# Kernel tuning notes

Hardware: AMD Instinct MI355X
Metric: run time of the kernel (lower is better)

Reference implementation:

```python
import jax, jax.numpy as jnp
import numpy as np

B, L, H, V = 16, 512, 256, 32000
HALF = H // 2
EPS_LN = 1e-5
EPS_NORM = 1e-12


def setup_inputs() -> dict:
    key = jax.random.key(0)
    ks = jax.random.split(key, 9)
    s = 0.02
    return {
        "seq": jax.random.randint(ks[0], (B, L), 0, V),
        "embed": jax.random.normal(ks[1], (V, H), jnp.float32) * s,
        "W1": jax.random.normal(ks[2], (2 * H, H), jnp.float32) * s,
        "b1": jnp.zeros((2 * H,), jnp.float32),
        "W2": jax.random.normal(ks[3], (H, 2 * H), jnp.float32) * s,
        "b2": jnp.zeros((H,), jnp.float32),
        "gamma": jnp.ones((H,), jnp.float32),
        "beta": jnp.zeros((H,), jnp.float32),
        "W_sem": jax.random.normal(ks[4], (HALF, H), jnp.float32) * s,
        "W_epi": jax.random.normal(ks[5], (HALF, H), jnp.float32) * s,
        "W_rp": jax.random.normal(ks[6], (H, H), jnp.float32) * s,
        "b_rp": jnp.zeros((H,), jnp.float32),
        "W_out": jax.random.normal(ks[7], (V, H), jnp.float32) * s,
        "b_out": jnp.zeros((V,), jnp.float32),
    }


def _l2norm(x):
    # F.normalize(dim=-1): x / max(||x||, eps)
    n = jnp.sqrt(jnp.sum(x * x, axis=-1, keepdims=True))
    return x / jnp.maximum(n, EPS_NORM)


def reference(seq, embed, W1, b1, W2, b2, gamma, beta, W_sem, W_epi, W_rp, b_rp, W_out, b_out):
    h = embed[seq]                                   # [B, L, H]
    ff = jnp.maximum(h @ W1.T + b1, 0.0) @ W2.T + b2  # MLP with 2H hidden
    x = h + ff
    mu = jnp.mean(x, axis=-1, keepdims=True)
    var = jnp.var(x, axis=-1, keepdims=True)
    h = (x - mu) / jnp.sqrt(var + EPS_LN) * gamma + beta  # LayerNorm

    ks_all = jnp.einsum('blh,kh->blk', h, W_sem)     # [B, L, HALF]
    ke_all = jnp.einsum('blh,kh->blk', h, W_epi)

    def step(carry, kv):
        M_s, M_e = carry
        k_s, k_e = kv                                 # [B, HALF] each
        kns = _l2norm(k_s)
        kne = _l2norm(k_e)
        vps = jnp.einsum('bij,bj->bi', M_s, kns)      # read from fast weights
        vpe = jnp.einsum('bij,bj->bi', M_e, kne)
        M_s = M_s + jnp.einsum('bi,bj->bij', k_s - vps, kns)  # delta-rule write
        M_e = M_e + jnp.einsum('bi,bj->bij', k_e - vpe, kne)
        return (M_s, M_e), None

    M0 = jnp.zeros((B, HALF, HALF), h.dtype)
    # scan over timesteps 0..L-2 (time-major)
    (M_s, M_e), _ = jax.lax.scan(
        step, (M0, M0),
        (jnp.swapaxes(ks_all[:, :-1], 0, 1), jnp.swapaxes(ke_all[:, :-1], 0, 1)))

    cs = jnp.einsum('bij,bj->bi', M_s, ks_all[:, -1])  # read with last-token query
    ce = jnp.einsum('bij,bj->bi', M_e, ke_all[:, -1])
    c = jnp.concatenate([cs, ce], axis=-1)             # [B, H]
    r = c @ W_rp.T + b_rp
    return r @ W_out.T + b_out                          # [B, V]
```

## Files before the change

### kernel.cpp

```cpp
#include <hip/hip_runtime.h>

#define B_ 16
#define L_ 512
#define H_ 256
#define V_ 32000
#define HALF_ 128

typedef __attribute__((ext_vector_type(8))) short short8;
typedef __attribute__((ext_vector_type(4))) float floatx4;
typedef __attribute__((ext_vector_type(2))) float float2v;

__device__ __forceinline__ unsigned short f2bf(float x) {
  unsigned int u = __float_as_uint(x);
  unsigned int r = (u + 0x7FFFu + ((u >> 16) & 1u)) >> 16;
  return (unsigned short)r;
}

template <int CTRL>
__device__ __forceinline__ float dpp_xor_add(float x) {
  int y = __builtin_amdgcn_mov_dpp(__float_as_int(x), CTRL, 0xf, 0xf, true);
  return x + __int_as_float(y);
}

__device__ __forceinline__ float redu16(float p) {
  p = dpp_xor_add<0xB1>(p);
  p = dpp_xor_add<0x4E>(p);
  p = dpp_xor_add<0x141>(p);
  p = dpp_xor_add<0x140>(p);
  return p;
}

__device__ __forceinline__ float2v pk_fma(float2v a, float2v b, float2v c) {
  float2v d;
  asm("v_pk_fma_f32 %0, %1, %2, %3" : "=v"(d) : "v"(a), "v"(b), "v"(c));
  return d;
}
__device__ __forceinline__ float2v pk_mul(float2v a, float2v b) {
  float2v d;
  asm("v_pk_mul_f32 %0, %1, %2" : "=v"(d) : "v"(a), "v"(b));
  return d;
}

__device__ __forceinline__ void async_cp16(const float* g, float* l) {
  __builtin_amdgcn_global_load_lds(
      (const __attribute__((address_space(1))) void*)g,
      (__attribute__((address_space(3))) void*)l, 16, 0, 0);
}

__device__ __forceinline__ uint4 load8cvt(const float* p) {
  float4 a = ((const float4*)p)[0];
  float4 b = ((const float4*)p)[1];
  uint4 r;
  r.x = (unsigned)f2bf(a.x) | ((unsigned)f2bf(a.y) << 16);
  r.y = (unsigned)f2bf(a.z) | ((unsigned)f2bf(a.w) << 16);
  r.z = (unsigned)f2bf(b.x) | ((unsigned)f2bf(b.y) << 16);
  r.w = (unsigned)f2bf(b.z) | ((unsigned)f2bf(b.w) << 16);
  return r;
}

__global__ __launch_bounds__(256) void prep_kernel(const float* __restrict__ W1,
                                                   const float* __restrict__ W2,
                                                   const float* __restrict__ Ws,
                                                   const float* __restrict__ We,
                                                   unsigned short* __restrict__ W1b,
                                                   unsigned short* __restrict__ W2b,
                                                   unsigned short* __restrict__ Wcb) {
  int i = blockIdx.x * 256 + threadIdx.x;
  if (i < 131072) W1b[i] = f2bf(W1[i]);
  else if (i < 262144) W2b[i - 131072] = f2bf(W2[i - 131072]);
  else if (i < 294912) Wcb[i - 262144] = f2bf(Ws[i - 262144]);
  else Wcb[i - 262144] = f2bf(We[i - 294912]);
}

__global__ __launch_bounds__(256) void gemm1_kernel(const int* __restrict__ seq,
                                                    const float* __restrict__ embed,
                                                    const unsigned short* __restrict__ W1b,
                                                    const float* __restrict__ b1,
                                                    unsigned short* __restrict__ a1b) {
  __shared__ unsigned short As[128 * 40];
  __shared__ unsigned short Bs[128 * 40];
  int tid = threadIdx.x;
  int wave = tid >> 6, lane = tid & 63;
  int wm = (wave >> 1) * 64, wn = (wave & 1) * 64;
  int quad = lane >> 4, l15 = lane & 15;
  int bm = blockIdx.y * 128, bn = blockIdx.x * 128;
  int sr = tid >> 2, sq = tid & 3;

  int tok0 = seq[bm + sr];
  int tok1 = seq[bm + 64 + sr];

  floatx4 zero = {0.f, 0.f, 0.f, 0.f};
  floatx4 acc[4][4];
#pragma unroll
  for (int fi = 0; fi < 4; fi++)
#pragma unroll
    for (int fj = 0; fj < 4; fj++) acc[fi][fj] = zero;

  uint4 av0 = load8cvt(embed + (size_t)tok0 * H_ + sq * 8);
  uint4 av1 = load8cvt(embed + (size_t)tok1 * H_ + sq * 8);
  uint4 bv0 = *(const uint4*)(W1b + (size_t)(bn + sr) * 256 + sq * 8);
  uint4 bv1 = *(const uint4*)(W1b + (size_t)(bn + 64 + sr) * 256 + sq * 8);

  for (int k0 = 0; k0 < 256; k0 += 32) {
    __syncthreads();
    *(uint4*)(As + sr * 40 + sq * 8) = av0;
    *(uint4*)(As + (64 + sr) * 40 + sq * 8) = av1;
    *(uint4*)(Bs + sr * 40 + sq * 8) = bv0;
    *(uint4*)(Bs + (64 + sr) * 40 + sq * 8) = bv1;
    __syncthreads();
    if (k0 + 32 < 256) {
      av0 = load8cvt(embed + (size_t)tok0 * H_ + k0 + 32 + sq * 8);
      av1 = load8cvt(embed + (size_t)tok1 * H_ + k0 + 32 + sq * 8);
      bv0 = *(const uint4*)(W1b + (size_t)(bn + sr) * 256 + k0 + 32 + sq * 8);
      bv1 = *(const uint4*)(W1b + (size_t)(bn + 64 + sr) * 256 + k0 + 32 + sq * 8);
    }
    short8 af[4], bf[4];
#pragma unroll
    for (int f = 0; f < 4; f++) {
      af[f] = *(const short8*)(As + (wm + f * 16 + l15) * 40 + quad * 8);
      bf[f] = *(const short8*)(Bs + (wn + f * 16 + l15) * 40 + quad * 8);
    }
#pragma unroll
    for (int fi = 0; fi < 4; fi++)
#pragma unroll
      for (int fj = 0; fj < 4; fj++)
        acc[fi][fj] = __builtin_amdgcn_mfma_f32_16x16x32_bf16(af[fi], bf[fj], acc[fi][fj], 0, 0, 0);
  }

#pragma unroll
  for (int fi = 0; fi < 4; fi++) {
#pragma unroll
    for (int fj = 0; fj < 4; fj++) {
      int col = bn + wn + fj * 16 + l15;
      float bb = b1[col];
#pragma unroll
      for (int rg = 0; rg < 4; rg++) {
        int row = bm + wm + fi * 16 + quad * 4 + rg;
        float v = fmaxf(acc[fi][fj][rg] + bb, 0.f);
        a1b[(size_t)row * 512 + col] = f2bf(v);
      }
    }
  }
}

__global__ __launch_bounds__(256) void mlpk_kernel(const unsigned short* __restrict__ a1b,
                                                   const unsigned short* __restrict__ W2b,
                                                   const float* __restrict__ b2,
                                                   const int* __restrict__ seq,
                                                   const float* __restrict__ embed,
                                                   const float* __restrict__ gamma,
                                                   const float* __restrict__ beta,
                                                   const unsigned short* __restrict__ Wcb,
                                                   float* __restrict__ khat,
                                                   float* __restrict__ kT) {
  __shared__ unsigned short As[32 * 40];
  __shared__ unsigned short Bs[256 * 40];
  __shared__ unsigned short hnS[32 * 264];
  __shared__ float stats[2][2][32];
  int tid = threadIdx.x;
  int wave = tid >> 6, lane = tid & 63;
  int wm = (wave >> 1) * 16, wnh = wave & 1, wn = wnh * 128;
  int quad = lane >> 4, l15 = lane & 15;
  int bm = blockIdx.x * 32;
  int sr = tid >> 2, sq = tid & 3;

  floatx4 zero = {0.f, 0.f, 0.f, 0.f};
  floatx4 acc[8];
#pragma unroll
  for (int fj = 0; fj < 8; fj++) acc[fj] = zero;

  uint4 av, bv[4];
  if (tid < 128) av = *(const uint4*)(a1b + (size_t)(bm + sr) * 512 + sq * 8);
#pragma unroll
  for (int q = 0; q < 4; q++) {
    int unit = q * 256 + tid;
    bv[q] = *(const uint4*)(W2b + (size_t)(unit >> 2) * 512 + (unit & 3) * 8);
  }
  for (int k0 = 0; k0 < 512; k0 += 32) {
    __syncthreads();
    if (tid < 128) *(uint4*)(As + sr * 40 + sq * 8) = av;
#pragma unroll
    for (int q = 0; q < 4; q++) {
      int unit = q * 256 + tid;
      *(uint4*)(Bs + (unit >> 2) * 40 + (unit & 3) * 8) = bv[q];
    }
    __syncthreads();
    if (k0 + 32 < 512) {
      if (tid < 128) av = *(const uint4*)(a1b + (size_t)(bm + sr) * 512 + k0 + 32 + sq * 8);
#pragma unroll
      for (int q = 0; q < 4; q++) {
        int unit = q * 256 + tid;
        bv[q] = *(const uint4*)(W2b + (size_t)(unit >> 2) * 512 + k0 + 32 + (unit & 3) * 8);
      }
    }
    short8 af = *(const short8*)(As + (wm + l15) * 40 + quad * 8);
    short8 bf[8];
#pragma unroll
    for (int fj = 0; fj < 8; fj++)
      bf[fj] = *(const short8*)(Bs + (wn + fj * 16 + l15) * 40 + quad * 8);
#pragma unroll
    for (int fj = 0; fj < 8; fj++)
      acc[fj] = __builtin_amdgcn_mfma_f32_16x16x32_bf16(af, bf[fj], acc[fj], 0, 0, 0);
  }

  int seqv[4];
#pragma unroll
  for (int rg = 0; rg < 4; rg++) seqv[rg] = seq[bm + wm + quad * 4 + rg];
  float v[8][4];
#pragma unroll
  for (int fj = 0; fj < 8; fj++) {
    int col = wn + fj * 16 + l15;
    float bb = b2[col];
#pragma unroll
    for (int rg = 0; rg < 4; rg++)
      v[fj][rg] = acc[fj][rg] + bb + embed[(size_t)seqv[rg] * H_ + col];
  }
  float s_[4], q_[4];
#pragma unroll
  for (int rg = 0; rg < 4; rg++) {
    float s = 0.f, q = 0.f;
#pragma unroll
    for (int fj = 0; fj < 8; fj++) {
      s += v[fj][rg];
      q += v[fj][rg] * v[fj][rg];
    }
    s_[rg] = redu16(s);
    q_[rg] = redu16(q);
  }
  if (l15 == 0) {
#pragma unroll
    for (int rg = 0; rg < 4; rg++) {
      int rlocal = wm + quad * 4 + rg;
      stats[wnh][0][rlocal] = s_[rg];
      stats[wnh][1][rlocal] = q_[rg];
    }
  }
  __syncthreads();
#pragma unroll
  for (int rg = 0; rg < 4; rg++) {
    int rlocal = wm + quad * 4 + rg;
    float sum = stats[0][0][rlocal] + stats[1][0][rlocal];
    float ssq = stats[0][1][rlocal] + stats[1][1][rlocal];
    float mu = sum * (1.f / H_);
    float var = ssq * (1.f / H_) - mu * mu;
    float inv = rsqrtf(var + 1e-5f);
#pragma unroll
    for (int fj = 0; fj < 8; fj++) {
      int col = wn + fj * 16 + l15;
      float y = (v[fj][rg] - mu) * inv * gamma[col] + beta[col];
      hnS[rlocal * 264 + col] = f2bf(y);
    }
  }
  __syncthreads();

  floatx4 acc2[8];
#pragma unroll
  for (int fj = 0; fj < 8; fj++) acc2[fj] = zero;
#pragma unroll
  for (int q = 0; q < 4; q++) {
    int unit = q * 256 + tid;
    bv[q] = *(const uint4*)(Wcb + (size_t)(unit >> 2) * 256 + (unit & 3) * 8);
  }
  for (int k0 = 0; k0 < 256; k0 += 32) {
    __syncthreads();
#pragma unroll
    for (int q = 0; q < 4; q++) {
      int unit = q * 256 + tid;
      *(uint4*)(Bs + (unit >> 2) * 40 + (unit & 3) * 8) = bv[q];
    }
    __syncthreads();
    if (k0 + 32 < 256) {
#pragma unroll
      for (int q = 0; q < 4; q++) {
        int unit = q * 256 + tid;
        bv[q] = *(const uint4*)(Wcb + (size_t)(unit >> 2) * 256 + k0 + 32 + (unit & 3) * 8);
      }
    }
    short8 af = *(const short8*)(hnS + (wm + l15) * 264 + k0 + quad * 8);
    short8 bf[8];
#pragma unroll
    for (int fj = 0; fj < 8; fj++)
      bf[fj] = *(const short8*)(Bs + (wn + fj * 16 + l15) * 40 + quad * 8);
#pragma unroll
    for (int fj = 0; fj < 8; fj++)
      acc2[fj] = __builtin_amdgcn_mfma_f32_16x16x32_bf16(af, bf[fj], acc2[fj], 0, 0, 0);
  }

  int b = bm >> 9;
  int idxm = b * 2 + wnh;
  int tloc0 = (bm & 511) + wm + quad * 4;
  float inv[4];
#pragma unroll
  for (int rg = 0; rg < 4; rg++) {
    float ssq = 0.f;
#pragma unroll
    for (int fj = 0; fj < 8; fj++) ssq += acc2[fj][rg] * acc2[fj][rg];
    ssq = redu16(ssq);
    inv[rg] = 1.f / fmaxf(sqrtf(ssq), 1e-12f);
  }
#pragma unroll
  for (int fj = 0; fj < 8; fj++) {
    int ch = fj * 16 + l15;
    int j = ch >> 2, e = ch & 3;
    int pj = (j & 1) ? (16 + (j >> 1)) : (j >> 1);
    int pcol = pj * 4 + e;
#pragma unroll
    for (int rg = 0; rg < 4; rg++)
      khat[((size_t)idxm * L_ + tloc0 + rg) * HALF_ + pcol] = acc2[fj][rg] * inv[rg];
    float4 raw = {acc2[fj][0], acc2[fj][1], acc2[fj][2], acc2[fj][3]};
    *(float4*)(kT + (size_t)idxm * (HALF_ * L_) + (size_t)ch * L_ + tloc0) = raw;
  }
}

#define STEP(KP, KR)                                                     \
  do {                                                                   \
    float2v t_ = pk_mul(m01, KP[0]);                                     \
    t_ = pk_fma(m23, KP[1], t_);                                         \
    t_ = pk_fma(m45, KP[2], t_);                                         \
    t_ = pk_fma(m67, KP[3], t_);                                         \
    float p_ = t_.x + t_.y;                                              \
    p_ = redu16(p_);                                                     \
    float sv_ = (KR) - p_;                                               \
    float2v s2_ = {sv_, sv_};                                            \
    m01 = pk_fma(s2_, KP[0], m01);                                       \
    m23 = pk_fma(s2_, KP[1], m23);                                       \
    m45 = pk_fma(s2_, KP[2], m45);                                       \
    m67 = pk_fma(s2_, KP[3], m67);                                       \
  } while (0)

#define LOADPK(DST, PTR)                                                 \
  do {                                                                   \
    float4 a_ = *(const float4*)(PTR);                                   \
    float4 b_ = *(const float4*)((PTR) + 64);                            \
    DST[0] = (float2v){a_.x, a_.y};                                      \
    DST[1] = (float2v){a_.z, a_.w};                                      \
    DST[2] = (float2v){b_.x, b_.y};                                      \
    DST[3] = (float2v){b_.z, b_.w};                                      \
  } while (0)

__global__ __launch_bounds__(256) void scan_kernel(const float* __restrict__ khat,
                                                   const float* __restrict__ kT,
                                                   float* __restrict__ c) {
  __shared__ float sk[2][64 * 128];
  int bid = blockIdx.x;
  int idxm = bid & 31;
  int rg = bid >> 5;
  int b = idxm >> 1, mat = idxm & 1;
  const float* kh = khat + (size_t)idxm * L_ * HALF_;
  const float* kTi = kT + (size_t)idxm * HALF_ * L_;

  int tid = threadIdx.x;
  int wave = tid >> 6, lane = tid & 63;
  int seg = tid & 15, rl = tid >> 4;
  int r = rg * 16 + rl;
  int c0 = seg * 8;
  const float* krow = kTi + (size_t)r * L_;

  float2v m01 = {0.f, 0.f}, m23 = {0.f, 0.f}, m45 = {0.f, 0.f}, m67 = {0.f, 0.f};

#pragma unroll
  for (int j = 0; j < 8; j++)
    async_cp16(kh + wave * 2048 + j * 256 + lane * 4, &sk[0][wave * 2048 + j * 256] + lane * 4);
  __syncthreads();

  float4 krn = *(const float4*)(krow);
  const float* lb = &sk[0][0] + seg * 4;

  for (int ch = 0; ch < 7; ch++) {
#pragma unroll
    for (int j = 0; j < 8; j++)
      async_cp16(kh + (size_t)(ch + 1) * 8192 + wave * 2048 + j * 256 + lane * 4,
                 &sk[(ch + 1) & 1][wave * 2048 + j * 256] + lane * 4);
    const float* base = lb + (ch & 1) * 8192;
    float2v pk[4][4];
#pragma unroll
    for (int u = 0; u < 4; u++) LOADPK(pk[u], base + u * 128);
    for (int g = 0; g < 15; g++) {
      float4 krc = krn;
      krn = *(const float4*)(krow + ch * 64 + g * 4 + 4);
#pragma unroll
      for (int u = 0; u < 4; u++) {
        STEP(pk[u], ((u == 0) ? krc.x : (u == 1) ? krc.y : (u == 2) ? krc.z : krc.w));
        int tn = g * 4 + u + 4;
        LOADPK(pk[u], base + tn * 128);
      }
    }
    {
      float4 krc = krn;
      krn = *(const float4*)(krow + ch * 64 + 64);
      STEP(pk[0], krc.x);
      STEP(pk[1], krc.y);
      STEP(pk[2], krc.z);
      STEP(pk[3], krc.w);
    }
    __syncthreads();
  }

  {
    const float* base = lb + 8192;
    float2v pk[4][4];
#pragma unroll
    for (int u = 0; u < 4; u++) LOADPK(pk[u], base + u * 128);
    for (int g = 0; g < 15; g++) {
      float4 krc = krn;
      krn = *(const float4*)(krow + 448 + g * 4 + 4);
#pragma unroll
      for (int u = 0; u < 4; u++) {
        STEP(pk[u], ((u == 0) ? krc.x : (u == 1) ? krc.y : (u == 2) ? krc.z : krc.w));
        int tn = g * 4 + u + 4;
        LOADPK(pk[u], base + tn * 128);
      }
    }
    float4 krc = krn;
    STEP(pk[0], krc.x);
    STEP(pk[1], krc.y);
    STEP(pk[2], krc.z);
  }

  float q[8];
#pragma unroll
  for (int j = 0; j < 8; j++) q[j] = kTi[(size_t)(c0 + j) * L_ + 511];
  float t0 = m01.x * q[0] + m01.y * q[1];
  float t1 = m23.x * q[2] + m23.y * q[3];
  float t2 = m45.x * q[4] + m45.y * q[5];
  float t3 = m67.x * q[6] + m67.y * q[7];
  float p = redu16((t0 + t1) + (t2 + t3));
  if (seg == 0) c[(size_t)b * H_ + mat * HALF_ + r] = p;
}

__global__ void rp_kernel(const float* __restrict__ c, const float* __restrict__ Wrp,
                          const float* __restrict__ brp, float* __restrict__ r) {
  int b = blockIdx.x;
  int n = threadIdx.x;
  __shared__ float cs[H_];
  cs[n] = c[(size_t)b * H_ + n];
  __syncthreads();
  const float4* w4 = (const float4*)(Wrp + (size_t)n * H_);
  const float4* c4 = (const float4*)cs;
  float acc = 0.f;
#pragma unroll 8
  for (int k = 0; k < H_ / 4; k++) {
    float4 w = w4[k], cc = c4[k];
    acc += w.x * cc.x + w.y * cc.y + w.z * cc.z + w.w * cc.w;
  }
  r[(size_t)b * H_ + n] = acc + brp[n];
}

__global__ __launch_bounds__(256) void out_kernel(const float* __restrict__ r,
                                                  const float* __restrict__ Wout,
                                                  const float* __restrict__ bout,
                                                  float* __restrict__ out) {
  __shared__ float rs[16 * 272];
  __shared__ float obuf[16 * 68];
  int tid = threadIdx.x;
#pragma unroll
  for (int q = 0; q < 16; q++) {
    int idx = q * 256 + tid;
    int bb = idx >> 8, cc = idx & 255;
    rs[bb * 272 + cc + 4 * (cc >> 6)] = r[idx];
  }
  __syncthreads();
  int row = tid >> 2, part = tid & 3;
  int v = blockIdx.x * 64 + row;
  const float4* w4 = (const float4*)(Wout + (size_t)v * H_ + part * 64);
  float acc[16];
#pragma unroll
  for (int bb = 0; bb < 16; bb++) acc[bb] = 0.f;
#pragma unroll 4
  for (int j = 0; j < 16; j++) {
    float4 w = w4[j];
#pragma unroll
    for (int bb = 0; bb < 16; bb++) {
      float4 rv = *(const float4*)&rs[bb * 272 + part * 68 + j * 4];
      acc[bb] += w.x * rv.x + w.y * rv.y + w.z * rv.z + w.w * rv.w;
    }
  }
  float bo = bout[v];
#pragma unroll
  for (int bb = 0; bb < 16; bb++) {
    acc[bb] = dpp_xor_add<0xB1>(acc[bb]);
    acc[bb] = dpp_xor_add<0x4E>(acc[bb]);
  }
#pragma unroll
  for (int q = 0; q < 4; q++) {
    int bb = part * 4 + q;
    obuf[bb * 68 + row] = acc[bb] + bo;
  }
  __syncthreads();
#pragma unroll
  for (int q = 0; q < 4; q++) {
    int idx = q * 256 + tid;
    int bb = idx >> 6, vl = idx & 63;
    out[(size_t)bb * V_ + blockIdx.x * 64 + vl] = obuf[bb * 68 + vl];
  }
}

extern "C" void kernel_launch(void* const* d_in, const int* in_sizes, int n_in,
                              void* d_out, int out_size, void* d_ws, size_t ws_size,
                              hipStream_t stream) {
  const int* seq = (const int*)d_in[0];
  const float* embed = (const float*)d_in[1];
  const float* W1 = (const float*)d_in[2];
  const float* b1 = (const float*)d_in[3];
  const float* W2 = (const float*)d_in[4];
  const float* b2 = (const float*)d_in[5];
  const float* gamma = (const float*)d_in[6];
  const float* beta = (const float*)d_in[7];
  const float* Wsem = (const float*)d_in[8];
  const float* Wepi = (const float*)d_in[9];
  const float* Wrp = (const float*)d_in[10];
  const float* brp = (const float*)d_in[11];
  const float* Wout = (const float*)d_in[12];
  const float* bout = (const float*)d_in[13];
  float* out = (float*)d_out;

  float* ws = (float*)d_ws;
  unsigned short* a1b = (unsigned short*)ws;
  float* khat = ws + 2097152;
  float* kT = ws + 4194304;
  unsigned short* W1b = (unsigned short*)(ws + 6291456);
  unsigned short* W2b = (unsigned short*)(ws + 6356992);
  unsigned short* Wcb = (unsigned short*)(ws + 6422528);
  float* c = ws + 6455296;
  float* r = ws + 6459392;

  prep_kernel<<<1280, 256, 0, stream>>>(W1, W2, Wsem, Wepi, W1b, W2b, Wcb);
  gemm1_kernel<<<dim3(4, 64), 256, 0, stream>>>(seq, embed, W1b, b1, a1b);
  mlpk_kernel<<<256, 256, 0, stream>>>(a1b, W2b, b2, seq, embed, gamma, beta, Wcb, khat, kT);
  scan_kernel<<<256, 256, 0, stream>>>(khat, kT, c);
  rp_kernel<<<16, 256, 0, stream>>>(c, Wrp, brp, r);
  out_kernel<<<500, 256, 0, stream>>>(r, Wout, bout, out);
}
```

Baseline: 231.4 us.

## Replace transposed raw-key buffer with per-token norms, rebuilding raw keys from normalized keys

The MLP kernel no longer writes a transposed copy of the unnormalized keys. It writes only the per-token L2 norm, and its normalized-key output now goes through shared memory so global stores are coalesced float4 rows. The scan kernel rebuilds the raw key as normalized key times norm, reading the normalized key from the shared tile it already loads. The final query read reuses the last normalized key scaled by its norm. This removes a large global write and the strided raw-key reads, in exchange for an extra LDS read per step and more shared memory in the MLP kernel.

```diff
diff --git a/kernel.cpp b/kernel.cpp
--- a/kernel.cpp
+++ b/kernel.cpp
@@ -152,11 +152,12 @@
                                                    const float* __restrict__ beta,
                                                    const unsigned short* __restrict__ Wcb,
                                                    float* __restrict__ khat,
-                                                   float* __restrict__ kT) {
+                                                   float* __restrict__ nrm) {
   __shared__ unsigned short As[32 * 40];
   __shared__ unsigned short Bs[256 * 40];
   __shared__ unsigned short hnS[32 * 264];
   __shared__ float stats[2][2][32];
+  __shared__ float stg[2][32 * 132];
   int tid = threadIdx.x;
   int wave = tid >> 6, lane = tid & 63;
   int wm = (wave >> 1) * 16, wnh = wave & 1, wn = wnh * 128;
@@ -289,14 +290,19 @@
   int b = bm >> 9;
   int idxm = b * 2 + wnh;
   int tloc0 = (bm & 511) + wm + quad * 4;
-  float inv[4];
+  float inv[4], nr4[4];
 #pragma unroll
   for (int rg = 0; rg < 4; rg++) {
     float ssq = 0.f;
 #pragma unroll
     for (int fj = 0; fj < 8; fj++) ssq += acc2[fj][rg] * acc2[fj][rg];
     ssq = redu16(ssq);
-    inv[rg] = 1.f / fmaxf(sqrtf(ssq), 1e-12f);
+    nr4[rg] = fmaxf(sqrtf(ssq), 1e-12f);
+    inv[rg] = 1.f / nr4[rg];
+  }
+  if (l15 == 0) {
+#pragma unroll
+    for (int rg = 0; rg < 4; rg++) nrm[(size_t)idxm * L_ + tloc0 + rg] = nr4[rg];
   }
 #pragma unroll
   for (int fj = 0; fj < 8; fj++) {
@@ -304,15 +310,24 @@
     int j = ch >> 2, e = ch & 3;
     int pj = (j & 1) ? (16 + (j >> 1)) : (j >> 1);
     int pcol = pj * 4 + e;
+    int trl = wm + quad * 4;
 #pragma unroll
     for (int rg = 0; rg < 4; rg++)
-      khat[((size_t)idxm * L_ + tloc0 + rg) * HALF_ + pcol] = acc2[fj][rg] * inv[rg];
-    float4 raw = {acc2[fj][0], acc2[fj][1], acc2[fj][2], acc2[fj][3]};
-    *(float4*)(kT + (size_t)idxm * (HALF_ * L_) + (size_t)ch * L_ + tloc0) = raw;
-  }
-}
-
-#define STEP(KP, KR)                                                     \
+      stg[wnh][(trl + rg) * 132 + pcol] = acc2[fj][rg] * inv[rg];
+  }
+  __syncthreads();
+#pragma unroll
+  for (int f = 0; f < 8; f++) {
+    int idx = f * 256 + tid;
+    int w = idx >> 10, rem = idx & 1023;
+    int tr = rem >> 5, l = rem & 31;
+    float4 vv = *(float4*)&stg[w][tr * 132 + l * 4];
+    int im = (bm >> 9) * 2 + w;
+    *(float4*)&khat[((size_t)im * L_ + (bm & 511) + tr) * HALF_ + l * 4] = vv;
+  }
+}
+
+#define STEP(KP, KH, NR)                                                 \
   do {                                                                   \
     float2v t_ = pk_mul(m01, KP[0]);                                     \
     t_ = pk_fma(m23, KP[1], t_);                                         \
@@ -320,7 +335,7 @@
     t_ = pk_fma(m67, KP[3], t_);                                         \
     float p_ = t_.x + t_.y;                                              \
     p_ = redu16(p_);                                                     \
-    float sv_ = (KR) - p_;                                               \
+    float sv_ = (KH) * (NR)-p_;                                          \
     float2v s2_ = {sv_, sv_};                                            \
     m01 = pk_fma(s2_, KP[0], m01);                                       \
     m23 = pk_fma(s2_, KP[1], m23);                                       \
@@ -339,7 +354,7 @@
   } while (0)
 
 __global__ __launch_bounds__(256) void scan_kernel(const float* __restrict__ khat,
-                                                   const float* __restrict__ kT,
+                                                   const float* __restrict__ nrm,
                                                    float* __restrict__ c) {
   __shared__ float sk[2][64 * 128];
   int bid = blockIdx.x;
@@ -347,14 +362,15 @@
   int rg = bid >> 5;
   int b = idxm >> 1, mat = idxm & 1;
   const float* kh = khat + (size_t)idxm * L_ * HALF_;
-  const float* kTi = kT + (size_t)idxm * HALF_ * L_;
+  const float* np = nrm + (size_t)idxm * L_;
 
   int tid = threadIdx.x;
   int wave = tid >> 6, lane = tid & 63;
   int seg = tid & 15, rl = tid >> 4;
   int r = rg * 16 + rl;
-  int c0 = seg * 8;
-  const float* krow = kTi + (size_t)r * L_;
+  int jj = r >> 2, ee = r & 3;
+  int pj = (jj & 1) ? (16 + (jj >> 1)) : (jj >> 1);
+  int prow = pj * 4 + ee;
 
   float2v m01 = {0.f, 0.f}, m23 = {0.f, 0.f}, m45 = {0.f, 0.f}, m67 = {0.f, 0.f};
 
@@ -363,8 +379,9 @@
     async_cp16(kh + wave * 2048 + j * 256 + lane * 4, &sk[0][wave * 2048 + j * 256] + lane * 4);
   __syncthreads();
 
-  float4 krn = *(const float4*)(krow);
+  float4 nrn = *(const float4*)(np);
   const float* lb = &sk[0][0] + seg * 4;
+  const float* lk = &sk[0][0] + prow;
 
   for (int ch = 0; ch < 7; ch++) {
 #pragma unroll
@@ -372,60 +389,68 @@
       async_cp16(kh + (size_t)(ch + 1) * 8192 + wave * 2048 + j * 256 + lane * 4,
                  &sk[(ch + 1) & 1][wave * 2048 + j * 256] + lane * 4);
     const float* base = lb + (ch & 1) * 8192;
+    const float* kb2 = lk + (ch & 1) * 8192;
     float2v pk[4][4];
-#pragma unroll
-    for (int u = 0; u < 4; u++) LOADPK(pk[u], base + u * 128);
+    float kh4[4];
+#pragma unroll
+    for (int u = 0; u < 4; u++) {
+      LOADPK(pk[u], base + u * 128);
+      kh4[u] = kb2[u * 128];
+    }
     for (int g = 0; g < 15; g++) {
-      float4 krc = krn;
-      krn = *(const float4*)(krow + ch * 64 + g * 4 + 4);
+      float4 nrc = nrn;
+      nrn = *(const float4*)(np + ch * 64 + g * 4 + 4);
 #pragma unroll
       for (int u = 0; u < 4; u++) {
-        STEP(pk[u], ((u == 0) ? krc.x : (u == 1) ? krc.y : (u == 2) ? krc.z : krc.w));
+        STEP(pk[u], kh4[u], ((u == 0) ? nrc.x : (u == 1) ? nrc.y : (u == 2) ? nrc.z : nrc.w));
         int tn = g * 4 + u + 4;
         LOADPK(pk[u], base + tn * 128);
+        kh4[u] = kb2[tn * 128];
       }
     }
     {
-      float4 krc = krn;
-      krn = *(const float4*)(krow + ch * 64 + 64);
-      STEP(pk[0], krc.x);
-      STEP(pk[1], krc.y);
-      STEP(pk[2], krc.z);
-      STEP(pk[3], krc.w);
+      float4 nrc = nrn;
+      nrn = *(const float4*)(np + ch * 64 + 64);
+      STEP(pk[0], kh4[0], nrc.x);
+      STEP(pk[1], kh4[1], nrc.y);
+      STEP(pk[2], kh4[2], nrc.z);
+      STEP(pk[3], kh4[3], nrc.w);
     }
     __syncthreads();
   }
 
   {
     const float* base = lb + 8192;
+    const float* kb2 = lk + 8192;
     float2v pk[4][4];
-#pragma unroll
-    for (int u = 0; u < 4; u++) LOADPK(pk[u], base + u * 128);
+    float kh4[4];
+#pragma unroll
+    for (int u = 0; u < 4; u++) {
+      LOADPK(pk[u], base + u * 128);
+      kh4[u] = kb2[u * 128];
+    }
     for (int g = 0; g < 15; g++) {
-      float4 krc = krn;
-      krn = *(const float4*)(krow + 448 + g * 4 + 4);
+      float4 nrc = nrn;
+      nrn = *(const float4*)(np + 448 + g * 4 + 4);
 #pragma unroll
       for (int u = 0; u < 4; u++) {
-        STEP(pk[u], ((u == 0) ? krc.x : (u == 1) ? krc.y : (u == 2) ? krc.z : krc.w));
+        STEP(pk[u], kh4[u], ((u == 0) ? nrc.x : (u == 1) ? nrc.y : (u == 2) ? nrc.z : nrc.w));
         int tn = g * 4 + u + 4;
         LOADPK(pk[u], base + tn * 128);
+        kh4[u] = kb2[tn * 128];
       }
     }
-    float4 krc = krn;
-    STEP(pk[0], krc.x);
-    STEP(pk[1], krc.y);
-    STEP(pk[2], krc.z);
-  }
-
-  float q[8];
-#pragma unroll
-  for (int j = 0; j < 8; j++) q[j] = kTi[(size_t)(c0 + j) * L_ + 511];
-  float t0 = m01.x * q[0] + m01.y * q[1];
-  float t1 = m23.x * q[2] + m23.y * q[3];
-  float t2 = m45.x * q[4] + m45.y * q[5];
-  float t3 = m67.x * q[6] + m67.y * q[7];
-  float p = redu16((t0 + t1) + (t2 + t3));
-  if (seg == 0) c[(size_t)b * H_ + mat * HALF_ + r] = p;
+    float4 nrc = nrn;
+    STEP(pk[0], kh4[0], nrc.x);
+    STEP(pk[1], kh4[1], nrc.y);
+    STEP(pk[2], kh4[2], nrc.z);
+    float2v tq = pk_mul(m01, pk[3][0]);
+    tq = pk_fma(m23, pk[3][1], tq);
+    tq = pk_fma(m45, pk[3][2], tq);
+    tq = pk_fma(m67, pk[3][3], tq);
+    float p = redu16(tq.x + tq.y) * nrc.w;
+    if (seg == 0) c[(size_t)b * H_ + mat * HALF_ + r] = p;
+  }
 }
 
 __global__ void rp_kernel(const float* __restrict__ c, const float* __restrict__ Wrp,
@@ -517,17 +542,17 @@
   float* ws = (float*)d_ws;
   unsigned short* a1b = (unsigned short*)ws;
   float* khat = ws + 2097152;
-  float* kT = ws + 4194304;
-  unsigned short* W1b = (unsigned short*)(ws + 6291456);
-  unsigned short* W2b = (unsigned short*)(ws + 6356992);
-  unsigned short* Wcb = (unsigned short*)(ws + 6422528);
-  float* c = ws + 6455296;
-  float* r = ws + 6459392;
+  float* nrm = ws + 4194304;
+  unsigned short* W1b = (unsigned short*)(ws + 4210688);
+  unsigned short* W2b = (unsigned short*)(ws + 4276224);
+  unsigned short* Wcb = (unsigned short*)(ws + 4341760);
+  float* c = ws + 4374528;
+  float* r = ws + 4378624;
 
   prep_kernel<<<1280, 256, 0, stream>>>(W1, W2, Wsem, Wepi, W1b, W2b, Wcb);
   gemm1_kernel<<<dim3(4, 64), 256, 0, stream>>>(seq, embed, W1b, b1, a1b);
-  mlpk_kernel<<<256, 256, 0, stream>>>(a1b, W2b, b2, seq, embed, gamma, beta, Wcb, khat, kT);
-  scan_kernel<<<256, 256, 0, stream>>>(khat, kT, c);
+  mlpk_kernel<<<256, 256, 0, stream>>>(a1b, W2b, b2, seq, embed, gamma, beta, Wcb, khat, nrm);
+  scan_kernel<<<256, 256, 0, stream>>>(khat, nrm, c);
   rp_kernel<<<16, 256, 0, stream>>>(c, Wrp, brp, r);
   out_kernel<<<500, 256, 0, stream>>>(r, Wout, bout, out);
 }
```

Result: no change. 231.6 us (+0.1%).
